# Performance work log

Measured on AMD Instinct MI355X. Metric: run time of the kernel, lower is better.

Reference implementation:

```python
import jax, jax.numpy as jnp
import numpy as np

B, L, H, E = 4, 2048, 8, 64
S, D = L, E  # causal mask forces L == S


def setup_inputs() -> dict:
    key = jax.random.key(0)
    kq, kk, kv, km = jax.random.split(key, 4)
    return {
        "queries": jax.random.normal(kq, (B, L, H, E), dtype=jnp.float32),
        "keys": jax.random.normal(kk, (B, S, H, E), dtype=jnp.float32),
        "values": jax.random.normal(kv, (B, S, H, D), dtype=jnp.float32),
        "map": jax.random.normal(km, (S, S), dtype=jnp.float32),
    }


def reference(queries, keys, values, map):
    # queries: [B,L,H,E], keys: [B,S,H,E], values: [B,S,H,D], map: [S,S]
    E_ = queries.shape[-1]
    scale = 1.0 / jnp.sqrt(jnp.asarray(E_, dtype=queries.dtype))
    # raw attention scores: [B,H,L,S]
    scores = jnp.einsum("blhe,bshe->bhls", queries, keys)
    # mix scores with learned map along the key axis: [B,H,L,S]
    scores = jnp.einsum("bhls,st->bhlt", scores, map)
    # causal mask (TriangularCausalMask: triu with diagonal=1 is masked)
    Lq = queries.shape[1]
    causal = jnp.triu(jnp.ones((Lq, Lq), dtype=bool), k=1)  # [L,S]
    scores = jnp.where(causal[None, None, :, :], -jnp.inf, scores)
    attn = jax.nn.softmax(scale * scores, axis=-1)  # dropout p=0.0 -> identity
    out = jnp.einsum("bhls,bshd->blhd", attn, values)  # [B,L,H,D]
    return out
```

## Files before the change

kernel.cpp:

```cpp
#include <hip/hip_runtime.h>


typedef short bf16x8 __attribute__((ext_vector_type(8)));
typedef float f32x4 __attribute__((ext_vector_type(4)));
typedef float f32x16 __attribute__((ext_vector_type(16)));
typedef unsigned short u16x8 __attribute__((ext_vector_type(8)));
typedef unsigned int u32x4 __attribute__((ext_vector_type(4)));

typedef __attribute__((address_space(1))) const void gvoid;
typedef __attribute__((address_space(3))) void lvoid;

__device__ __forceinline__ unsigned short f2bf(float x) {
  unsigned int u = __float_as_uint(x);
  u += 0x7FFFu + ((u >> 16) & 1u);
  return (unsigned short)(u >> 16);
}
__device__ __forceinline__ float bf2f(unsigned short h) {
  return __uint_as_float(((unsigned int)h) << 16);
}
__device__ __forceinline__ unsigned int cvtpk(float lo, float hi) {
  unsigned int r;
  asm("v_cvt_pk_bf16_f32 %0, %1, %2" : "=v"(r) : "v"(lo), "v"(hi));
  return r;
}

__device__ __forceinline__ void gload16(const unsigned short* g, unsigned short* l) {
  __builtin_amdgcn_global_load_lds((gvoid*)g, (lvoid*)l, 16, 0, 0);
}

__device__ __forceinline__ void stage_tile(const unsigned short* __restrict__ g,
                                           int gstride, unsigned short* l,
                                           int rows, int tid) {
  const int lane = tid & 63, w = tid >> 6;
  const int nch = rows << 3;
  for (int c0 = (w << 6); c0 < nch; c0 += 256) {
    const int c = c0 + lane;
    const int row = c >> 3;
    const int bir = (c & 7) << 4;
    const int sb = bir ^ ((row & 7) << 4);
    gload16(g + (size_t)row * gstride + (sb >> 1), l + (size_t)c0 * 8);
  }
}

__device__ __forceinline__ int swz(int row, int byteInRow) {
  return row * 128 + (byteInRow ^ ((row & 7) << 4));
}

__global__ __launch_bounds__(256) void prep_m(const float* __restrict__ M,
                                              unsigned short* __restrict__ Mh,
                                              unsigned short* __restrict__ Ml) {
  __shared__ float Ts[64][68];
  const int s0 = blockIdx.x << 6, t0 = blockIdx.y << 6;
  const int tid = threadIdx.x, r = tid >> 2, c0 = (tid & 3) << 4;
  const float* src = M + (size_t)(s0 + r) * 2048 + t0 + c0;
#pragma unroll
  for (int j = 0; j < 4; ++j)
    *(float4*)&Ts[r][c0 + 4 * j] = *(const float4*)(src + 4 * j);
  __syncthreads();
  u16x8 h0, h1, l0v, l1v;
#pragma unroll
  for (int j = 0; j < 8; ++j) {
    float x = Ts[c0 + j][r];
    unsigned short hh = f2bf(x);
    h0[j] = hh; l0v[j] = f2bf(x - bf2f(hh));
  }
#pragma unroll
  for (int j = 8; j < 16; ++j) {
    float x = Ts[c0 + j][r];
    unsigned short hh = f2bf(x);
    h1[j - 8] = hh; l1v[j - 8] = f2bf(x - bf2f(hh));
  }
  const size_t o = (size_t)(t0 + r) * 2048 + s0 + c0;
  *(u16x8*)(Mh + o) = h0; *(u16x8*)(Mh + o + 8) = h1;
  *(u16x8*)(Ml + o) = l0v; *(u16x8*)(Ml + o + 8) = l1v;
}

__global__ __launch_bounds__(256) void prep_kv(const float* __restrict__ src4d,
                                               unsigned short* __restrict__ Dh,
                                               unsigned short* __restrict__ Dl,
                                               int has_lo) {
  __shared__ float Ts[64][68];
  const int s0 = blockIdx.x << 6, bh = blockIdx.y;
  const int b = bh >> 3, h = bh & 7;
  const int tid = threadIdx.x, r = tid >> 2, c0 = (tid & 3) << 4;
  const float* src = src4d + ((size_t)(b * 2048 + s0 + r) * 8 + h) * 64 + c0;
#pragma unroll
  for (int j = 0; j < 4; ++j)
    *(float4*)&Ts[r][c0 + 4 * j] = *(const float4*)(src + 4 * j);
  __syncthreads();
  u16x8 h0, h1, l0v, l1v;
#pragma unroll
  for (int j = 0; j < 8; ++j) {
    float x = Ts[c0 + j][r];
    unsigned short hh = f2bf(x);
    h0[j] = hh; l0v[j] = f2bf(x - bf2f(hh));
  }
#pragma unroll
  for (int j = 8; j < 16; ++j) {
    float x = Ts[c0 + j][r];
    unsigned short hh = f2bf(x);
    h1[j - 8] = hh; l1v[j - 8] = f2bf(x - bf2f(hh));
  }
  const size_t o = ((size_t)bh * 64 + r) * 2048 + s0 + c0;
  *(u16x8*)(Dh + o) = h0; *(u16x8*)(Dh + o + 8) = h1;
  if (has_lo) { *(u16x8*)(Dl + o) = l0v; *(u16x8*)(Dl + o + 8) = l1v; }
}

__global__ __launch_bounds__(256) void km_mfma(
    const unsigned short* __restrict__ Mth, const unsigned short* __restrict__ Mtl,
    const unsigned short* __restrict__ Kth, const unsigned short* __restrict__ Ktl,
    unsigned short* __restrict__ KMh, unsigned short* __restrict__ KMl) {
  __shared__ __attribute__((aligned(16))) unsigned short sm[24576];
  unsigned short* MtH = sm;
  unsigned short* MtL = sm + 8192;
  unsigned short* KtH = sm + 16384;
  unsigned short* KtL = sm + 20480;
  const int tid = threadIdx.x, lane = tid & 63, w = tid >> 6;
  const int g = lane >> 4, li = lane & 15;
  const int t0 = blockIdx.x << 7;
  const int bh = blockIdx.y;
  const unsigned short* KtHb = Kth + (size_t)bh * 64 * 2048;
  const unsigned short* KtLb = Ktl + (size_t)bh * 64 * 2048;

  f32x4 acc[2][4];
#pragma unroll
  for (int mi = 0; mi < 2; ++mi)
#pragma unroll
    for (int ni = 0; ni < 4; ++ni) acc[mi][ni] = (f32x4){0.f, 0.f, 0.f, 0.f};

  for (int s0 = 0; s0 < 2048; s0 += 64) {
    __syncthreads();
    stage_tile(Mth + (size_t)t0 * 2048 + s0, 2048, MtH, 128, tid);
    stage_tile(Mtl + (size_t)t0 * 2048 + s0, 2048, MtL, 128, tid);
    stage_tile(KtHb + s0, 2048, KtH, 64, tid);
    stage_tile(KtLb + s0, 2048, KtL, 64, tid);
    asm volatile("s_waitcnt vmcnt(0)" ::: "memory");
    __syncthreads();
#pragma unroll
    for (int kk = 0; kk < 2; ++kk) {
      const int kb = (kk * 32 + 8 * g) * 2;
      bf16x8 aH[2], aL[2];
#pragma unroll
      for (int mi = 0; mi < 2; ++mi) {
        const int row = (w << 5) + (mi << 4) + li;
        aH[mi] = *(const bf16x8*)((const char*)MtH + swz(row, kb));
        aL[mi] = *(const bf16x8*)((const char*)MtL + swz(row, kb));
      }
#pragma unroll
      for (int ni = 0; ni < 4; ++ni) {
        const int row = (ni << 4) + li;
        const int off = swz(row, kb);
        const bf16x8 bH = *(const bf16x8*)((const char*)KtH + off);
        const bf16x8 bL = *(const bf16x8*)((const char*)KtL + off);
#pragma unroll
        for (int mi = 0; mi < 2; ++mi) {
          acc[mi][ni] = __builtin_amdgcn_mfma_f32_16x16x32_bf16(aH[mi], bH, acc[mi][ni], 0, 0, 0);
          acc[mi][ni] = __builtin_amdgcn_mfma_f32_16x16x32_bf16(aH[mi], bL, acc[mi][ni], 0, 0, 0);
          acc[mi][ni] = __builtin_amdgcn_mfma_f32_16x16x32_bf16(aL[mi], bH, acc[mi][ni], 0, 0, 0);
        }
      }
    }
  }
  const size_t base = (size_t)bh * 2048 * 64;
#pragma unroll
  for (int mi = 0; mi < 2; ++mi)
#pragma unroll
    for (int r = 0; r < 4; ++r) {
      const int trow = t0 + (w << 5) + (mi << 4) + (g << 2) + r;
#pragma unroll
      for (int ni = 0; ni < 4; ++ni) {
        const float x = acc[mi][ni][r];
        const unsigned short hh = f2bf(x);
        const size_t idx = base + (size_t)trow * 64 + (ni << 4) + li;
        KMh[idx] = hh;
        KMl[idx] = f2bf(x - bf2f(hh));
      }
    }
}

__global__ __launch_bounds__(256, 2) void attn32(
    const float* __restrict__ Q, const unsigned short* __restrict__ KMh,
    const unsigned short* __restrict__ KMl, const unsigned short* __restrict__ Vt,
    float* __restrict__ Out) {
  __shared__ __attribute__((aligned(16))) unsigned short sm[24576];
  const int tid = threadIdx.x, lane = tid & 63, w = tid >> 6;
  const int g2 = lane >> 5, li5 = lane & 31;

  const int bid = (int)blockIdx.x;
  const int x = bid & 7;
  const int r = bid >> 3;
  const int m = r >> 2;
  const int bh = (x << 2) | (r & 3);
  const int lt = (m < 8) ? (15 - m) : (m - 8);
  const int b = bh >> 3, h = bh & 7;
  const int l0 = lt << 7;
  const int qg = l0 + (w << 5) + li5;

  const float SC2 = 0.18033688011112042f;
  bf16x8 qh[4], ql[4];
  {
    const float* qsrc = Q + (((size_t)(b * 2048 + qg) * 8 + h) << 6) + (g2 << 3);
#pragma unroll
    for (int kk = 0; kk < 4; ++kk) {
      const float4 v0 = *(const float4*)(qsrc + 16 * kk);
      const float4 v1 = *(const float4*)(qsrc + 16 * kk + 4);
      const float xs[8] = {v0.x, v0.y, v0.z, v0.w, v1.x, v1.y, v1.z, v1.w};
#pragma unroll
      for (int j = 0; j < 8; ++j) {
        const float xv = xs[j] * SC2;
        const unsigned short hh = f2bf(xv);
        qh[kk][j] = (short)hh;
        ql[kk][j] = (short)f2bf(xv - bf2f(hh));
      }
    }
  }

  f32x16 o0 = {0,0,0,0,0,0,0,0,0,0,0,0,0,0,0,0};
  f32x16 o1 = {0,0,0,0,0,0,0,0,0,0,0,0,0,0,0,0};
  f32x16 lsacc = {0,0,0,0,0,0,0,0,0,0,0,0,0,0,0,0};
  float m2 = -1e30f;
  bf16x8 ones;
#pragma unroll
  for (int j = 0; j < 8; ++j) ones[j] = (short)0x3F80;

  const unsigned short* KHb = KMh + (size_t)bh * 2048 * 64;
  const unsigned short* KLb = KMl + (size_t)bh * 2048 * 64;
  const unsigned short* VTb = Vt + (size_t)bh * 64 * 2048;

  const int jtmax_blk = 2 * lt + 1;
  const int jtmax_w = 2 * lt + (w >> 1);

  {
    unsigned short* s0b = sm;
    stage_tile(KHb, 64, s0b, 64, tid);
    stage_tile(KLb, 64, s0b + 4096, 64, tid);
    stage_tile(VTb, 2048, s0b + 8192, 64, tid);
  }
  asm volatile("s_waitcnt vmcnt(0)" ::: "memory");
  __builtin_amdgcn_s_barrier();
  __builtin_amdgcn_sched_barrier(0);

  for (int jt = 0; jt <= jtmax_blk; ++jt) {
    const int cur = jt & 1;
    if (jt < jtmax_blk) {
      unsigned short* nb = sm + (cur ^ 1) * 12288;
      stage_tile(KHb + (size_t)(jt + 1) * 4096, 64, nb, 64, tid);
      stage_tile(KLb + (size_t)(jt + 1) * 4096, 64, nb + 4096, 64, tid);
      stage_tile(VTb + (jt + 1) * 64, 2048, nb + 8192, 64, tid);
    }

    if (jt <= jtmax_w) {
      const unsigned short* KH = sm + cur * 12288;
      const unsigned short* KL = KH + 4096;
      const unsigned short* VT = KH + 8192;

      f32x16 z0 = {0,0,0,0,0,0,0,0,0,0,0,0,0,0,0,0};
      f32x16 z1 = {0,0,0,0,0,0,0,0,0,0,0,0,0,0,0,0};
      __builtin_amdgcn_s_setprio(1);
#pragma unroll
      for (int kk = 0; kk < 4; ++kk) {
        const int cb = 32 * kk + 16 * g2;
        const bf16x8 a0h = *(const bf16x8*)((const char*)KH + swz(li5, cb));
        const bf16x8 a0l = *(const bf16x8*)((const char*)KL + swz(li5, cb));
        const bf16x8 a1h = *(const bf16x8*)((const char*)KH + swz(32 + li5, cb));
        const bf16x8 a1l = *(const bf16x8*)((const char*)KL + swz(32 + li5, cb));
        z0 = __builtin_amdgcn_mfma_f32_32x32x16_bf16(a0h, qh[kk], z0, 0, 0, 0);
        z0 = __builtin_amdgcn_mfma_f32_32x32x16_bf16(a0h, ql[kk], z0, 0, 0, 0);
        z0 = __builtin_amdgcn_mfma_f32_32x32x16_bf16(a0l, qh[kk], z0, 0, 0, 0);
        z1 = __builtin_amdgcn_mfma_f32_32x32x16_bf16(a1h, qh[kk], z1, 0, 0, 0);
        z1 = __builtin_amdgcn_mfma_f32_32x32x16_bf16(a1h, ql[kk], z1, 0, 0, 0);
        z1 = __builtin_amdgcn_mfma_f32_32x32x16_bf16(a1l, qh[kk], z1, 0, 0, 0);
      }
      __builtin_amdgcn_s_setprio(0);

      const bool needmask = (jt * 64 + 63 > l0 + (w << 5));
      if (needmask) {
        const int thr = qg - jt * 64;
#pragma unroll
        for (int rr = 0; rr < 16; ++rr) {
          const int tl = (g2 << 2) + ((rr >> 2) << 3) + (rr & 3);
          if (tl > thr) z0[rr] = -1e30f;
          if (tl + 32 > thr) z1[rr] = -1e30f;
        }
      }

      float t16[16];
#pragma unroll
      for (int rr = 0; rr < 16; ++rr) t16[rr] = fmaxf(z0[rr], z1[rr]);
#pragma unroll
      for (int s = 8; s; s >>= 1)
#pragma unroll
        for (int rr = 0; rr < 8; ++rr)
          if (rr < s) t16[rr] = fmaxf(t16[rr], t16[rr + s]);
      const float mx = fmaxf(t16[0], __shfl_xor(t16[0], 32));
      if (__any(mx > m2 + 11.0f)) {
        const float m2n = fmaxf(m2, mx);
        const float fs = exp2f(m2 - m2n);
        m2 = m2n;
#pragma unroll
        for (int rr = 0; rr < 16; ++rr) { o0[rr] *= fs; o1[rr] *= fs; }
        lsacc[0] *= fs;
      }

      float pv0[16], pv1[16];
#pragma unroll
      for (int rr = 0; rr < 16; ++rr) {
        pv0[rr] = exp2f(z0[rr] - m2);
        pv1[rr] = exp2f(z1[rr] - m2);
      }
      unsigned int W0[8], W1[8];
#pragma unroll
      for (int i = 0; i < 8; ++i) {
        W0[i] = cvtpk(pv0[2 * i], pv0[2 * i + 1]);
        W1[i] = cvtpk(pv1[2 * i], pv1[2 * i + 1]);
      }
      asm volatile("v_permlane32_swap_b32 %0, %1" : "+v"(W0[0]), "+v"(W0[2]));
      asm volatile("v_permlane32_swap_b32 %0, %1" : "+v"(W0[1]), "+v"(W0[3]));
      asm volatile("v_permlane32_swap_b32 %0, %1" : "+v"(W0[4]), "+v"(W0[6]));
      asm volatile("v_permlane32_swap_b32 %0, %1" : "+v"(W0[5]), "+v"(W0[7]));
      asm volatile("v_permlane32_swap_b32 %0, %1" : "+v"(W1[0]), "+v"(W1[2]));
      asm volatile("v_permlane32_swap_b32 %0, %1" : "+v"(W1[1]), "+v"(W1[3]));
      asm volatile("v_permlane32_swap_b32 %0, %1" : "+v"(W1[4]), "+v"(W1[6]));
      asm volatile("v_permlane32_swap_b32 %0, %1" : "+v"(W1[5]), "+v"(W1[7]));
      bf16x8 pf[4];
      {
        u32x4 f0 = {W0[0], W0[1], W0[2], W0[3]};
        u32x4 f1 = {W0[4], W0[5], W0[6], W0[7]};
        u32x4 f2 = {W1[0], W1[1], W1[2], W1[3]};
        u32x4 f3 = {W1[4], W1[5], W1[6], W1[7]};
        pf[0] = __builtin_bit_cast(bf16x8, f0);
        pf[1] = __builtin_bit_cast(bf16x8, f1);
        pf[2] = __builtin_bit_cast(bf16x8, f2);
        pf[3] = __builtin_bit_cast(bf16x8, f3);
      }

      __builtin_amdgcn_s_setprio(1);
#pragma unroll
      for (int kk = 0; kk < 4; ++kk) {
        const int cb = 32 * kk + 16 * g2;
        const bf16x8 v0f = *(const bf16x8*)((const char*)VT + swz(li5, cb));
        const bf16x8 v1f = *(const bf16x8*)((const char*)VT + swz(32 + li5, cb));
        o0 = __builtin_amdgcn_mfma_f32_32x32x16_bf16(v0f, pf[kk], o0, 0, 0, 0);
        o1 = __builtin_amdgcn_mfma_f32_32x32x16_bf16(v1f, pf[kk], o1, 0, 0, 0);
        lsacc = __builtin_amdgcn_mfma_f32_32x32x16_bf16(ones, pf[kk], lsacc, 0, 0, 0);
      }
      __builtin_amdgcn_s_setprio(0);
    }

    asm volatile("s_waitcnt vmcnt(0)" ::: "memory");
    __builtin_amdgcn_s_barrier();
    __builtin_amdgcn_sched_barrier(0);
  }

  const float inv = 1.f / lsacc[0];
  float* ob = Out + (((size_t)(b * 2048 + qg) * 8 + h) << 6);
#pragma unroll
  for (int r2 = 0; r2 < 4; ++r2) {
    const int doff = (g2 << 2) + (r2 << 3);
    float4 s0 = make_float4(o0[4 * r2] * inv, o0[4 * r2 + 1] * inv,
                            o0[4 * r2 + 2] * inv, o0[4 * r2 + 3] * inv);
    *(float4*)(ob + doff) = s0;
    float4 s1 = make_float4(o1[4 * r2] * inv, o1[4 * r2 + 1] * inv,
                            o1[4 * r2 + 2] * inv, o1[4 * r2 + 3] * inv);
    *(float4*)(ob + 32 + doff) = s1;
  }
}

extern "C" void kernel_launch(void* const* d_in, const int* in_sizes, int n_in,
                              void* d_out, int out_size, void* d_ws, size_t ws_size,
                              hipStream_t stream) {
  const float* Q = (const float*)d_in[0];
  const float* K = (const float*)d_in[1];
  const float* V = (const float*)d_in[2];
  const float* M = (const float*)d_in[3];
  float* Out = (float*)d_out;
  char* ws = (char*)d_ws;
  const size_t MB = 1u << 20;
  unsigned short* Mth = (unsigned short*)(ws);
  unsigned short* Mtl = (unsigned short*)(ws + 8 * MB);
  unsigned short* Kth = (unsigned short*)(ws + 16 * MB);
  unsigned short* Ktl = (unsigned short*)(ws + 24 * MB);
  unsigned short* Vts = (unsigned short*)(ws + 32 * MB);
  unsigned short* KMh = (unsigned short*)(ws + 40 * MB);
  unsigned short* KMl = (unsigned short*)(ws + 48 * MB);

  prep_m<<<dim3(32, 32), 256, 0, stream>>>(M, Mth, Mtl);
  prep_kv<<<dim3(32, 32), 256, 0, stream>>>(K, Kth, Ktl, 1);
  prep_kv<<<dim3(32, 32), 256, 0, stream>>>(V, Vts, (unsigned short*)nullptr, 0);
  km_mfma<<<dim3(16, 32), 256, 0, stream>>>(Mth, Mtl, Kth, Ktl, KMh, KMl);
  attn32<<<dim3(512), 256, 0, stream>>>(Q, KMh, KMl, Vts, Out);
}
```

Before: 147.5 us.

## Split long causal query tiles across two blocks and retile K·M GEMM

```diff
diff --git a/kernel.cpp b/kernel.cpp
--- a/kernel.cpp
+++ b/kernel.cpp
@@ -28,12 +28,13 @@
   __builtin_amdgcn_global_load_lds((gvoid*)g, (lvoid*)l, 16, 0, 0);
 }
 
+template <int NW>
 __device__ __forceinline__ void stage_tile(const unsigned short* __restrict__ g,
                                            int gstride, unsigned short* l,
                                            int rows, int tid) {
   const int lane = tid & 63, w = tid >> 6;
   const int nch = rows << 3;
-  for (int c0 = (w << 6); c0 < nch; c0 += 256) {
+  for (int c0 = (w << 6); c0 < nch; c0 += NW * 64) {
     const int c = c0 + lane;
     const int row = c >> 3;
     const int bir = (c & 7) << 4;
@@ -106,111 +107,152 @@
   if (has_lo) { *(u16x8*)(Dl + o) = l0v; *(u16x8*)(Dl + o + 8) = l1v; }
 }
 
-__global__ __launch_bounds__(256) void km_mfma(
+__global__ __launch_bounds__(512, 2) void km_mfma2(
     const unsigned short* __restrict__ Mth, const unsigned short* __restrict__ Mtl,
     const unsigned short* __restrict__ Kth, const unsigned short* __restrict__ Ktl,
     unsigned short* __restrict__ KMh, unsigned short* __restrict__ KMl) {
-  __shared__ __attribute__((aligned(16))) unsigned short sm[24576];
-  unsigned short* MtH = sm;
-  unsigned short* MtL = sm + 8192;
-  unsigned short* KtH = sm + 16384;
-  unsigned short* KtL = sm + 20480;
+  __shared__ __attribute__((aligned(16))) unsigned short sm[40960];
+  unsigned short* MH = sm;
+  unsigned short* ML = sm + 16384;
+  unsigned short* KH = sm + 32768;
+  unsigned short* KL = sm + 36864;
   const int tid = threadIdx.x, lane = tid & 63, w = tid >> 6;
-  const int g = lane >> 4, li = lane & 15;
-  const int t0 = blockIdx.x << 7;
-  const int bh = blockIdx.y;
-  const unsigned short* KtHb = Kth + (size_t)bh * 64 * 2048;
-  const unsigned short* KtLb = Ktl + (size_t)bh * 64 * 2048;
-
-  f32x4 acc[2][4];
-#pragma unroll
-  for (int mi = 0; mi < 2; ++mi)
-#pragma unroll
-    for (int ni = 0; ni < 4; ++ni) acc[mi][ni] = (f32x4){0.f, 0.f, 0.f, 0.f};
+  const int g2 = lane >> 5, li5 = lane & 31;
+  const int tc = w & 3, sh = w >> 2;
+
+  const int x = (int)blockIdx.x & 7;
+  const int bh = (int)blockIdx.x >> 3;
+  const int t0 = x << 8;
+
+  const unsigned short* MthB = Mth + (size_t)t0 * 2048;
+  const unsigned short* MtlB = Mtl + (size_t)t0 * 2048;
+  const unsigned short* KthB = Kth + (size_t)bh * 64 * 2048;
+  const unsigned short* KtlB = Ktl + (size_t)bh * 64 * 2048;
+
+  f32x16 acc[2][2];
+#pragma unroll
+  for (int tf = 0; tf < 2; ++tf)
+#pragma unroll
+    for (int ef = 0; ef < 2; ++ef)
+      acc[tf][ef] = (f32x16){0,0,0,0,0,0,0,0,0,0,0,0,0,0,0,0};
 
   for (int s0 = 0; s0 < 2048; s0 += 64) {
     __syncthreads();
-    stage_tile(Mth + (size_t)t0 * 2048 + s0, 2048, MtH, 128, tid);
-    stage_tile(Mtl + (size_t)t0 * 2048 + s0, 2048, MtL, 128, tid);
-    stage_tile(KtHb + s0, 2048, KtH, 64, tid);
-    stage_tile(KtLb + s0, 2048, KtL, 64, tid);
+    stage_tile<8>(MthB + s0, 2048, MH, 256, tid);
+    stage_tile<8>(MtlB + s0, 2048, ML, 256, tid);
+    stage_tile<8>(KthB + s0, 2048, KH, 64, tid);
+    stage_tile<8>(KtlB + s0, 2048, KL, 64, tid);
     asm volatile("s_waitcnt vmcnt(0)" ::: "memory");
     __syncthreads();
-#pragma unroll
-    for (int kk = 0; kk < 2; ++kk) {
-      const int kb = (kk * 32 + 8 * g) * 2;
-      bf16x8 aH[2], aL[2];
-#pragma unroll
-      for (int mi = 0; mi < 2; ++mi) {
-        const int row = (w << 5) + (mi << 4) + li;
-        aH[mi] = *(const bf16x8*)((const char*)MtH + swz(row, kb));
-        aL[mi] = *(const bf16x8*)((const char*)MtL + swz(row, kb));
-      }
-#pragma unroll
-      for (int ni = 0; ni < 4; ++ni) {
-        const int row = (ni << 4) + li;
-        const int off = swz(row, kb);
-        const bf16x8 bH = *(const bf16x8*)((const char*)KtH + off);
-        const bf16x8 bL = *(const bf16x8*)((const char*)KtL + off);
-#pragma unroll
-        for (int mi = 0; mi < 2; ++mi) {
-          acc[mi][ni] = __builtin_amdgcn_mfma_f32_16x16x32_bf16(aH[mi], bH, acc[mi][ni], 0, 0, 0);
-          acc[mi][ni] = __builtin_amdgcn_mfma_f32_16x16x32_bf16(aH[mi], bL, acc[mi][ni], 0, 0, 0);
-          acc[mi][ni] = __builtin_amdgcn_mfma_f32_16x16x32_bf16(aL[mi], bH, acc[mi][ni], 0, 0, 0);
+
+    __builtin_amdgcn_s_setprio(1);
+#pragma unroll
+    for (int kg = 0; kg < 2; ++kg) {
+      const int kb = ((sh << 1) + kg) * 32 + (g2 << 4);
+      const int ra0 = (tc << 6) + li5;
+      const bf16x8 aH0 = *(const bf16x8*)((const char*)MH + swz(ra0, kb));
+      const bf16x8 aL0 = *(const bf16x8*)((const char*)ML + swz(ra0, kb));
+      const bf16x8 aH1 = *(const bf16x8*)((const char*)MH + swz(ra0 + 32, kb));
+      const bf16x8 aL1 = *(const bf16x8*)((const char*)ML + swz(ra0 + 32, kb));
+      const bf16x8 bH0 = *(const bf16x8*)((const char*)KH + swz(li5, kb));
+      const bf16x8 bL0 = *(const bf16x8*)((const char*)KL + swz(li5, kb));
+      const bf16x8 bH1 = *(const bf16x8*)((const char*)KH + swz(32 + li5, kb));
+      const bf16x8 bL1 = *(const bf16x8*)((const char*)KL + swz(32 + li5, kb));
+      acc[0][0] = __builtin_amdgcn_mfma_f32_32x32x16_bf16(aH0, bH0, acc[0][0], 0, 0, 0);
+      acc[0][0] = __builtin_amdgcn_mfma_f32_32x32x16_bf16(aH0, bL0, acc[0][0], 0, 0, 0);
+      acc[0][0] = __builtin_amdgcn_mfma_f32_32x32x16_bf16(aL0, bH0, acc[0][0], 0, 0, 0);
+      acc[0][1] = __builtin_amdgcn_mfma_f32_32x32x16_bf16(aH0, bH1, acc[0][1], 0, 0, 0);
+      acc[0][1] = __builtin_amdgcn_mfma_f32_32x32x16_bf16(aH0, bL1, acc[0][1], 0, 0, 0);
+      acc[0][1] = __builtin_amdgcn_mfma_f32_32x32x16_bf16(aL0, bH1, acc[0][1], 0, 0, 0);
+      acc[1][0] = __builtin_amdgcn_mfma_f32_32x32x16_bf16(aH1, bH0, acc[1][0], 0, 0, 0);
+      acc[1][0] = __builtin_amdgcn_mfma_f32_32x32x16_bf16(aH1, bL0, acc[1][0], 0, 0, 0);
+      acc[1][0] = __builtin_amdgcn_mfma_f32_32x32x16_bf16(aL1, bH0, acc[1][0], 0, 0, 0);
+      acc[1][1] = __builtin_amdgcn_mfma_f32_32x32x16_bf16(aH1, bH1, acc[1][1], 0, 0, 0);
+      acc[1][1] = __builtin_amdgcn_mfma_f32_32x32x16_bf16(aH1, bL1, acc[1][1], 0, 0, 0);
+      acc[1][1] = __builtin_amdgcn_mfma_f32_32x32x16_bf16(aL1, bH1, acc[1][1], 0, 0, 0);
+    }
+    __builtin_amdgcn_s_setprio(0);
+  }
+
+  __syncthreads();
+  float* red = (float*)sm;
+  if (sh == 1) {
+#pragma unroll
+    for (int tf = 0; tf < 2; ++tf)
+#pragma unroll
+      for (int ef = 0; ef < 2; ++ef) {
+        const int fi = (tc << 2) | (tf << 1) | ef;
+        float* dst = red + (size_t)(fi * 64 + lane) * 17;
+#pragma unroll
+        for (int rr = 0; rr < 16; ++rr) dst[rr] = acc[tf][ef][rr];
+      }
+  }
+  __syncthreads();
+  if (sh == 0) {
+    const size_t base = (size_t)bh * (2048 * 64);
+#pragma unroll
+    for (int tf = 0; tf < 2; ++tf)
+#pragma unroll
+      for (int ef = 0; ef < 2; ++ef) {
+        const int fi = (tc << 2) | (tf << 1) | ef;
+        const float* src = red + (size_t)(fi * 64 + lane) * 17;
+#pragma unroll
+        for (int rr = 0; rr < 16; ++rr) {
+          const float v = acc[tf][ef][rr] + src[rr];
+          const int trow = t0 + (tc << 6) + (tf << 5) + (g2 << 2) +
+                           ((rr >> 2) << 3) + (rr & 3);
+          const int e = (ef << 5) + li5;
+          const unsigned short hh = f2bf(v);
+          const size_t idx = base + (size_t)trow * 64 + e;
+          KMh[idx] = hh;
+          KMl[idx] = f2bf(v - bf2f(hh));
         }
       }
-    }
-  }
-  const size_t base = (size_t)bh * 2048 * 64;
-#pragma unroll
-  for (int mi = 0; mi < 2; ++mi)
-#pragma unroll
-    for (int r = 0; r < 4; ++r) {
-      const int trow = t0 + (w << 5) + (mi << 4) + (g << 2) + r;
-#pragma unroll
-      for (int ni = 0; ni < 4; ++ni) {
-        const float x = acc[mi][ni][r];
-        const unsigned short hh = f2bf(x);
-        const size_t idx = base + (size_t)trow * 64 + (ni << 4) + li;
-        KMh[idx] = hh;
-        KMl[idx] = f2bf(x - bf2f(hh));
-      }
-    }
-}
-
-__global__ __launch_bounds__(256, 2) void attn32(
+  }
+}
+
+__global__ __launch_bounds__(256, 3) void attn32(
     const float* __restrict__ Q, const unsigned short* __restrict__ KMh,
     const unsigned short* __restrict__ KMl, const unsigned short* __restrict__ Vt,
-    float* __restrict__ Out) {
+    float* __restrict__ Out, float* __restrict__ Opart, float* __restrict__ Ml) {
   __shared__ __attribute__((aligned(16))) unsigned short sm[24576];
   const int tid = threadIdx.x, lane = tid & 63, w = tid >> 6;
   const int g2 = lane >> 5, li5 = lane & 31;
 
   const int bid = (int)blockIdx.x;
-  const int x = bid & 7;
-  const int r = bid >> 3;
-  const int m = r >> 2;
-  const int bh = (x << 2) | (r & 3);
-  const int lt = (m < 8) ? (15 - m) : (m - 8);
+  const int x = bid & 7, n = bid >> 3;
+  const int slot = n >> 5, j = n & 31;
+  const int bh = (x << 2) | (j & 3);
+  const int kk = j >> 2;
+  int lt, jt0, jtEnd;
+  bool partial;
+  if (slot == 2) {
+    lt = kk; jt0 = 0; jtEnd = 2 * kk + 1; partial = false;
+  } else {
+    lt = 15 - kk;
+    const int half = 16 - kk;
+    jt0 = slot * half; jtEnd = jt0 + half - 1; partial = true;
+  }
   const int b = bh >> 3, h = bh & 7;
   const int l0 = lt << 7;
   const int qg = l0 + (w << 5) + li5;
+  const int rloc = (w << 5) + li5;
 
   const float SC2 = 0.18033688011112042f;
   bf16x8 qh[4], ql[4];
   {
     const float* qsrc = Q + (((size_t)(b * 2048 + qg) * 8 + h) << 6) + (g2 << 3);
 #pragma unroll
-    for (int kk = 0; kk < 4; ++kk) {
-      const float4 v0 = *(const float4*)(qsrc + 16 * kk);
-      const float4 v1 = *(const float4*)(qsrc + 16 * kk + 4);
+    for (int kki = 0; kki < 4; ++kki) {
+      const float4 v0 = *(const float4*)(qsrc + 16 * kki);
+      const float4 v1 = *(const float4*)(qsrc + 16 * kki + 4);
       const float xs[8] = {v0.x, v0.y, v0.z, v0.w, v1.x, v1.y, v1.z, v1.w};
 #pragma unroll
-      for (int j = 0; j < 8; ++j) {
-        const float xv = xs[j] * SC2;
+      for (int jj = 0; jj < 8; ++jj) {
+        const float xv = xs[jj] * SC2;
         const unsigned short hh = f2bf(xv);
-        qh[kk][j] = (short)hh;
-        ql[kk][j] = (short)f2bf(xv - bf2f(hh));
+        qh[kki][jj] = (short)hh;
+        ql[kki][jj] = (short)f2bf(xv - bf2f(hh));
       }
     }
   }
@@ -221,32 +263,31 @@
   float m2 = -1e30f;
   bf16x8 ones;
 #pragma unroll
-  for (int j = 0; j < 8; ++j) ones[j] = (short)0x3F80;
+  for (int jj = 0; jj < 8; ++jj) ones[jj] = (short)0x3F80;
 
   const unsigned short* KHb = KMh + (size_t)bh * 2048 * 64;
   const unsigned short* KLb = KMl + (size_t)bh * 2048 * 64;
   const unsigned short* VTb = Vt + (size_t)bh * 64 * 2048;
 
-  const int jtmax_blk = 2 * lt + 1;
   const int jtmax_w = 2 * lt + (w >> 1);
 
   {
-    unsigned short* s0b = sm;
-    stage_tile(KHb, 64, s0b, 64, tid);
-    stage_tile(KLb, 64, s0b + 4096, 64, tid);
-    stage_tile(VTb, 2048, s0b + 8192, 64, tid);
+    unsigned short* s0b = sm + (jt0 & 1) * 12288;
+    stage_tile<4>(KHb + (size_t)jt0 * 4096, 64, s0b, 64, tid);
+    stage_tile<4>(KLb + (size_t)jt0 * 4096, 64, s0b + 4096, 64, tid);
+    stage_tile<4>(VTb + jt0 * 64, 2048, s0b + 8192, 64, tid);
   }
   asm volatile("s_waitcnt vmcnt(0)" ::: "memory");
   __builtin_amdgcn_s_barrier();
   __builtin_amdgcn_sched_barrier(0);
 
-  for (int jt = 0; jt <= jtmax_blk; ++jt) {
+  for (int jt = jt0; jt <= jtEnd; ++jt) {
     const int cur = jt & 1;
-    if (jt < jtmax_blk) {
+    if (jt < jtEnd) {
       unsigned short* nb = sm + (cur ^ 1) * 12288;
-      stage_tile(KHb + (size_t)(jt + 1) * 4096, 64, nb, 64, tid);
-      stage_tile(KLb + (size_t)(jt + 1) * 4096, 64, nb + 4096, 64, tid);
-      stage_tile(VTb + (jt + 1) * 64, 2048, nb + 8192, 64, tid);
+      stage_tile<4>(KHb + (size_t)(jt + 1) * 4096, 64, nb, 64, tid);
+      stage_tile<4>(KLb + (size_t)(jt + 1) * 4096, 64, nb + 4096, 64, tid);
+      stage_tile<4>(VTb + (jt + 1) * 64, 2048, nb + 8192, 64, tid);
     }
 
     if (jt <= jtmax_w) {
@@ -258,18 +299,18 @@
       f32x16 z1 = {0,0,0,0,0,0,0,0,0,0,0,0,0,0,0,0};
       __builtin_amdgcn_s_setprio(1);
 #pragma unroll
-      for (int kk = 0; kk < 4; ++kk) {
-        const int cb = 32 * kk + 16 * g2;
+      for (int kki = 0; kki < 4; ++kki) {
+        const int cb = 32 * kki + 16 * g2;
         const bf16x8 a0h = *(const bf16x8*)((const char*)KH + swz(li5, cb));
         const bf16x8 a0l = *(const bf16x8*)((const char*)KL + swz(li5, cb));
         const bf16x8 a1h = *(const bf16x8*)((const char*)KH + swz(32 + li5, cb));
         const bf16x8 a1l = *(const bf16x8*)((const char*)KL + swz(32 + li5, cb));
-        z0 = __builtin_amdgcn_mfma_f32_32x32x16_bf16(a0h, qh[kk], z0, 0, 0, 0);
-        z0 = __builtin_amdgcn_mfma_f32_32x32x16_bf16(a0h, ql[kk], z0, 0, 0, 0);
-        z0 = __builtin_amdgcn_mfma_f32_32x32x16_bf16(a0l, qh[kk], z0, 0, 0, 0);
-        z1 = __builtin_amdgcn_mfma_f32_32x32x16_bf16(a1h, qh[kk], z1, 0, 0, 0);
-        z1 = __builtin_amdgcn_mfma_f32_32x32x16_bf16(a1h, ql[kk], z1, 0, 0, 0);
-        z1 = __builtin_amdgcn_mfma_f32_32x32x16_bf16(a1l, qh[kk], z1, 0, 0, 0);
+        z0 = __builtin_amdgcn_mfma_f32_32x32x16_bf16(a0h, qh[kki], z0, 0, 0, 0);
+        z0 = __builtin_amdgcn_mfma_f32_32x32x16_bf16(a0h, ql[kki], z0, 0, 0, 0);
+        z0 = __builtin_amdgcn_mfma_f32_32x32x16_bf16(a0l, qh[kki], z0, 0, 0, 0);
+        z1 = __builtin_amdgcn_mfma_f32_32x32x16_bf16(a1h, qh[kki], z1, 0, 0, 0);
+        z1 = __builtin_amdgcn_mfma_f32_32x32x16_bf16(a1h, ql[kki], z1, 0, 0, 0);
+        z1 = __builtin_amdgcn_mfma_f32_32x32x16_bf16(a1l, qh[kki], z1, 0, 0, 0);
       }
       __builtin_amdgcn_s_setprio(0);
 
@@ -336,13 +377,13 @@
 
       __builtin_amdgcn_s_setprio(1);
 #pragma unroll
-      for (int kk = 0; kk < 4; ++kk) {
-        const int cb = 32 * kk + 16 * g2;
+      for (int kki = 0; kki < 4; ++kki) {
+        const int cb = 32 * kki + 16 * g2;
         const bf16x8 v0f = *(const bf16x8*)((const char*)VT + swz(li5, cb));
         const bf16x8 v1f = *(const bf16x8*)((const char*)VT + swz(32 + li5, cb));
-        o0 = __builtin_amdgcn_mfma_f32_32x32x16_bf16(v0f, pf[kk], o0, 0, 0, 0);
-        o1 = __builtin_amdgcn_mfma_f32_32x32x16_bf16(v1f, pf[kk], o1, 0, 0, 0);
-        lsacc = __builtin_amdgcn_mfma_f32_32x32x16_bf16(ones, pf[kk], lsacc, 0, 0, 0);
+        o0 = __builtin_amdgcn_mfma_f32_32x32x16_bf16(v0f, pf[kki], o0, 0, 0, 0);
+        o1 = __builtin_amdgcn_mfma_f32_32x32x16_bf16(v1f, pf[kki], o1, 0, 0, 0);
+        lsacc = __builtin_amdgcn_mfma_f32_32x32x16_bf16(ones, pf[kki], lsacc, 0, 0, 0);
       }
       __builtin_amdgcn_s_setprio(0);
     }
@@ -352,18 +393,68 @@
     __builtin_amdgcn_sched_barrier(0);
   }
 
-  const float inv = 1.f / lsacc[0];
-  float* ob = Out + (((size_t)(b * 2048 + qg) * 8 + h) << 6);
-#pragma unroll
-  for (int r2 = 0; r2 < 4; ++r2) {
-    const int doff = (g2 << 2) + (r2 << 3);
-    float4 s0 = make_float4(o0[4 * r2] * inv, o0[4 * r2 + 1] * inv,
-                            o0[4 * r2 + 2] * inv, o0[4 * r2 + 3] * inv);
-    *(float4*)(ob + doff) = s0;
-    float4 s1 = make_float4(o1[4 * r2] * inv, o1[4 * r2 + 1] * inv,
-                            o1[4 * r2 + 2] * inv, o1[4 * r2 + 3] * inv);
-    *(float4*)(ob + 32 + doff) = s1;
-  }
+  if (!partial) {
+    const float inv = 1.f / lsacc[0];
+    float* ob = Out + (((size_t)(b * 2048 + qg) * 8 + h) << 6);
+#pragma unroll
+    for (int r2 = 0; r2 < 4; ++r2) {
+      const int doff = (g2 << 2) + (r2 << 3);
+      float4 s0 = make_float4(o0[4 * r2] * inv, o0[4 * r2 + 1] * inv,
+                              o0[4 * r2 + 2] * inv, o0[4 * r2 + 3] * inv);
+      *(float4*)(ob + doff) = s0;
+      float4 s1 = make_float4(o1[4 * r2] * inv, o1[4 * r2 + 1] * inv,
+                              o1[4 * r2 + 2] * inv, o1[4 * r2 + 3] * inv);
+      *(float4*)(ob + 32 + doff) = s1;
+    }
+  } else {
+    const size_t pidx = (((size_t)slot * 32 + bh) * 8 + kk) * 128 + rloc;
+    float* op = Opart + pidx * 64;
+#pragma unroll
+    for (int r2 = 0; r2 < 4; ++r2) {
+      const int doff = (g2 << 2) + (r2 << 3);
+      *(float4*)(op + doff) =
+          make_float4(o0[4 * r2], o0[4 * r2 + 1], o0[4 * r2 + 2], o0[4 * r2 + 3]);
+      *(float4*)(op + 32 + doff) =
+          make_float4(o1[4 * r2], o1[4 * r2 + 1], o1[4 * r2 + 2], o1[4 * r2 + 3]);
+    }
+    Ml[pidx * 2] = m2;
+    Ml[pidx * 2 + 1] = lsacc[0];
+  }
+}
+
+__global__ __launch_bounds__(256) void attn_combine(
+    const float* __restrict__ Opart, const float* __restrict__ Ml,
+    float* __restrict__ Out) {
+  const int tid = threadIdx.x;
+  const int rowg = (int)blockIdx.x * 32 + (tid >> 3);
+  const int d0 = (tid & 7) << 3;
+  const int r = rowg & 127, kk = (rowg >> 7) & 7, bh = rowg >> 10;
+  const int b = bh >> 3, h = bh & 7;
+  const int lt = 15 - kk;
+  const size_t pidx = (((size_t)bh * 8 + kk) * 128 + r);
+  const size_t PSLOT = (size_t)32 * 8 * 128 * 64;
+  const size_t MSLOT = (size_t)32 * 8 * 128 * 2;
+  const float m0 = Ml[pidx * 2], ls0 = Ml[pidx * 2 + 1];
+  const float m1 = Ml[MSLOT + pidx * 2], ls1 = Ml[MSLOT + pidx * 2 + 1];
+  const float mm = fmaxf(m0, m1);
+  const float w0 = exp2f(m0 - mm), w1 = exp2f(m1 - mm);
+  const float inv = 1.f / (ls0 * w0 + ls1 * w1);
+  const float* p0 = Opart + pidx * 64 + d0;
+  const float* p1 = Opart + PSLOT + pidx * 64 + d0;
+  const float4 a0 = *(const float4*)(p0);
+  const float4 a1 = *(const float4*)(p0 + 4);
+  const float4 b0 = *(const float4*)(p1);
+  const float4 b1 = *(const float4*)(p1 + 4);
+  const int qg = lt * 128 + r;
+  float* o = Out + (((size_t)(b * 2048 + qg) * 8 + h) << 6) + d0;
+  *(float4*)o = make_float4((a0.x * w0 + b0.x * w1) * inv,
+                            (a0.y * w0 + b0.y * w1) * inv,
+                            (a0.z * w0 + b0.z * w1) * inv,
+                            (a0.w * w0 + b0.w * w1) * inv);
+  *(float4*)(o + 4) = make_float4((a1.x * w0 + b1.x * w1) * inv,
+                                  (a1.y * w0 + b1.y * w1) * inv,
+                                  (a1.z * w0 + b1.z * w1) * inv,
+                                  (a1.w * w0 + b1.w * w1) * inv);
 }
 
 extern "C" void kernel_launch(void* const* d_in, const int* in_sizes, int n_in,
@@ -383,10 +474,13 @@
   unsigned short* Vts = (unsigned short*)(ws + 32 * MB);
   unsigned short* KMh = (unsigned short*)(ws + 40 * MB);
   unsigned short* KMl = (unsigned short*)(ws + 48 * MB);
+  float* Opart = (float*)(ws);
+  float* Mlp = (float*)(ws + 16 * MB);
 
   prep_m<<<dim3(32, 32), 256, 0, stream>>>(M, Mth, Mtl);
   prep_kv<<<dim3(32, 32), 256, 0, stream>>>(K, Kth, Ktl, 1);
   prep_kv<<<dim3(32, 32), 256, 0, stream>>>(V, Vts, (unsigned short*)nullptr, 0);
-  km_mfma<<<dim3(16, 32), 256, 0, stream>>>(Mth, Mtl, Kth, Ktl, KMh, KMl);
-  attn32<<<dim3(512), 256, 0, stream>>>(Q, KMh, KMl, Vts, Out);
-}
+  km_mfma2<<<dim3(256), 512, 0, stream>>>(Mth, Mtl, Kth, Ktl, KMh, KMl);
+  attn32<<<dim3(768), 256, 0, stream>>>(Q, KMh, KMl, Vts, Out, Opart, Mlp);
+  attn_combine<<<dim3(1024), 256, 0, stream>>>(Opart, Mlp, Out);
+}
```

New measurement: 167.7 us. 13.7% more time.
